# Optimization experiments

Hardware: AMD Instinct MI355X
Metric: run time of the kernel (lower is better)

## Reference

```python
import jax, jax.numpy as jnp
import numpy as np

# pywt db4 reconstruction low-pass (rec_lo) coefficients.
_H = np.array([
    0.23037781330885523, 0.7148465705525415, 0.6308807679295904,
    -0.02798376941698385, -0.18703481171888114, 0.030841381835986965,
    0.032883011666982945, -0.010597401784997278], dtype=np.float64)
# pywt dec_lo = _H[::-1]; conv (flipped) correlation kernel = dec_lo[::-1] = _H.
_FLO = _H
# dec_hi[k] = (-1)^(7-k) * _H[k]; correlation kernel = dec_hi[::-1] -> (-1)^k * _H[7-k].
_FHI = np.array([(-1.0) ** k * _H[7 - k] for k in range(8)])
_FILT = jnp.asarray(np.stack([_FLO, _FHI])[:, None, :], dtype=jnp.float32)  # [2,1,8]
_PAD = 7  # filter_len - 1
_LEVEL = 4


def _dwt_step(sig):
    """One pywt dwt level, mode='symmetric'. sig: [N, L] -> (cA, cD), each [N, (L+7)//2]."""
    # symmetric (half-sample) extension by filter_len-1 each side, drop first sample
    # so that stride-2 VALID correlation reproduces pywt's output phase/length.
    xp = jnp.pad(sig, ((0, 0), (_PAD, _PAD)), mode='symmetric')[:, 1:]
    out = jax.lax.conv_general_dilated(
        xp[:, None, :], _FILT, window_strides=(2,), padding='VALID',
        dimension_numbers=('NCH', 'OIH', 'NCH'))  # [N, 2, (L+7)//2]
    return out[:, 0, :], out[:, 1, :]


def setup_inputs() -> dict:
    key = jax.random.key(0)
    x = jax.random.normal(key, (64, 4096, 32), dtype=jnp.float32)  # [B, L, C]
    return {"x": x}


def reference(x):
    """Faithful batched version of pywt.wavedec(x[i,:,j], 'db4', 'symmetric', level=4).
    Returns tuple (cA4, cD4, cD3, cD2, cD1), each [B, C, scale_len]."""
    B, L, C = x.shape
    sig = jnp.transpose(x, (0, 2, 1)).reshape(B * C, L)
    details = []
    for _ in range(_LEVEL):
        sig, cd = _dwt_step(sig)
        details.append(cd)
    coeffs = [sig] + details[::-1]  # [cA_L, cD_L, ..., cD_1] like pywt.wavedec
    return tuple(c.reshape(B, C, c.shape[-1]) for c in coeffs)
```

## Files before the change

kernel.cpp:

```cpp
#include <hip/hip_runtime.h>


#define NT 256
#define NCHB 4

#define LPX 634
#define LP1 322
#define LP2 166
#define LP3 86
#define CDP1 314
#define CDP2 154
#define CDP3 82
#define CDP4 40
#define CAP4 40

#define L0C 4096
#define L1C 2051
#define L2C 1029
#define L3C 518
#define L4C 262
#define SC 2048

#define OFF_CD4 (SC * L4C)
#define OFF_CD3 (2 * SC * L4C)
#define OFF_CD2 (OFF_CD3 + SC * L3C)
#define OFF_CD1 (OFF_CD2 + SC * L2C)

__device__ __forceinline__ void filt8(
    const float w0, const float w1, const float w2, const float w3,
    const float w4, const float w5, const float w6, const float w7,
    float& a, float& d) {
    constexpr float FLO[8] = {
        0.23037781330885523f,  0.7148465705525415f,  0.6308807679295904f,
        -0.02798376941698385f, -0.18703481171888114f, 0.030841381835986965f,
        0.032883011666982945f, -0.010597401784997278f};
    constexpr float FHI[8] = {
        -0.010597401784997278f, -0.032883011666982945f, 0.030841381835986965f,
        0.18703481171888114f,  -0.02798376941698385f,  -0.6308807679295904f,
        0.7148465705525415f,   -0.23037781330885523f};
    float a0 = FLO[0] * w0;
    a0 = fmaf(FLO[1], w1, a0); a0 = fmaf(FLO[2], w2, a0); a0 = fmaf(FLO[3], w3, a0);
    float a1 = FLO[4] * w4;
    a1 = fmaf(FLO[5], w5, a1); a1 = fmaf(FLO[6], w6, a1); a1 = fmaf(FLO[7], w7, a1);
    a = a0 + a1;
    float d0 = FHI[0] * w0;
    d0 = fmaf(FHI[1], w1, d0); d0 = fmaf(FHI[2], w2, d0); d0 = fmaf(FHI[3], w3, d0);
    float d1 = FHI[4] * w4;
    d1 = fmaf(FHI[5], w5, d1); d1 = fmaf(FHI[6], w6, d1); d1 = fmaf(FHI[7], w7, d1);
    d = d0 + d1;
}

template <int R, bool MG, bool LAST>
__device__ __forceinline__ void level_run(
    const float* __restrict__ src, int PS, int srclo,
    float* __restrict__ dst, int PD, int DL,
    int lo, int hi,
    float* __restrict__ cdbuf, int CDP,
    float* __restrict__ cabuf,
    int c, int slot) {
    static_assert((R & 1) == 0, "R must be even");
    const int span = hi - lo;
    const int nrun = span / R;
    bool tail = false;
    int i0;
    if (slot < nrun) {
        i0 = lo + slot * R;
    } else if (slot == nrun && nrun * R < span) {
        i0 = lo + ((span - R) & ~1);
        tail = (span & 1) != 0;
    } else {
        return;
    }

    const float* rowb = src + c * PS;
    const float2* row2 = reinterpret_cast<const float2*>(rowb);
    const int p = i0 - (srclo >> 1);
    float2 f0 = row2[p], f1 = row2[p + 1], f2 = row2[p + 2];

    float* dbase = LAST ? nullptr : dst + c * PD;
    float* cdbase = cdbuf + c * CDP;
    float* cabase = LAST ? cabuf + c * CAP4 : nullptr;

    float ap = 0.f, dp = 0.f;
#pragma unroll
    for (int r = 0; r < R; ++r) {
        const float2 f3 = row2[p + 3 + r];
        const int i = i0 + r;
        float a, d;
        filt8(f0.x, f0.y, f1.x, f1.y, f2.x, f2.y, f3.x, f3.y, a, d);
        if (r & 1) {
            const int w = i - 1 - lo;
            if constexpr (!LAST)
                *reinterpret_cast<float2*>(dbase + w + 6) = make_float2(ap, a);
            else
                *reinterpret_cast<float2*>(cabase + w) = make_float2(ap, a);
            *reinterpret_cast<float2*>(cdbase + w) = make_float2(dp, d);
        } else {
            ap = a; dp = d;
        }
        if constexpr (MG && !LAST) {
            if (lo == 0 && i < 6) dbase[5 - i] = a;
            if (hi == DL && i >= DL - 7) dbase[(2 * DL - 1 - i) - lo + 6] = a;
        }
        f0 = f1; f1 = f2; f2 = f3;
    }
    if (tail) {
        const int i = hi - 1;
        const float* s = rowb + 6 - srclo;
        float a, d;
        filt8(s[2*i-6], s[2*i-5], s[2*i-4], s[2*i-3],
              s[2*i-2], s[2*i-1], s[2*i],   s[2*i+1], a, d);
        if constexpr (!LAST) {
            dbase[i - lo + 6] = a;
            if constexpr (MG) {
                if (hi == DL && i >= DL - 7) dbase[(2 * DL - 1 - i) - lo + 6] = a;
            }
        } else {
            cabase[i - lo] = a;
        }
        cdbase[i - lo] = d;
    }
}

__device__ __forceinline__ void dump_rows(
    const float* __restrict__ buf, int pitch, int bufLo,
    float* __restrict__ gbase, int rowLen, int ownLo, int ownHi, int tid) {
    const int span = ownHi - ownLo;
    const int n2 = span >> 1;
    const int off = ownLo - bufLo;
#pragma unroll
    for (int c2 = 0; c2 < NCHB; ++c2) {
        const float2* s2 = reinterpret_cast<const float2*>(buf + c2 * pitch + off);
        float* g = gbase + c2 * rowLen + ownLo;
        for (int k = tid; k < n2; k += NT) {
            const float2 v = s2[k];
            g[2 * k] = v.x;
            g[2 * k + 1] = v.y;
        }
        if ((span & 1) && tid == 0) g[span - 1] = buf[c2 * pitch + off + span - 1];
    }
}

template <bool MG>
__device__ __forceinline__ void cascade(
    const float* bx, float* b1, float* b2, float* b3,
    float* cd1, float* cd2, float* cd3, float* cd4, float* ca4,
    float* __restrict__ out, int sigB, int tile, int c, int slot, int tid,
    int lox, int lo1, int hi1, int lo2, int hi2, int lo3, int hi3,
    int lo4, int hi4) {
    const int o1lo = tile ? 264 * tile - 34 : 0;
    const int o1hi = (tile == 7) ? L1C : 264 * tile + 230;
    const int o2lo = tile ? 132 * tile - 10 : 0;
    const int o2hi = (tile == 7) ? L2C : 132 * tile + 122;
    const int o3lo = tile ? 66 * tile - 2 : 0;
    const int o3hi = (tile == 7) ? L3C : 66 * tile + 64;

    level_run<6, MG, false>(bx, LPX, lox, b1, LP1, L1C, lo1, hi1, cd1, CDP1,
                            nullptr, c, slot);
    __syncthreads();

    dump_rows(cd1, CDP1, lo1, out + OFF_CD1 + sigB * L1C, L1C, o1lo, o1hi, tid);
    level_run<4, MG, false>(b1, LP1, lo1, b2, LP2, L2C, lo2, hi2, cd2, CDP2,
                            nullptr, c, slot);
    __syncthreads();

    dump_rows(cd2, CDP2, lo2, out + OFF_CD2 + sigB * L2C, L2C, o2lo, o2hi, tid);
    level_run<2, MG, false>(b2, LP2, lo2, b3, LP3, L3C, lo3, hi3, cd3, CDP3,
                            nullptr, c, slot);
    __syncthreads();

    dump_rows(cd3, CDP3, lo3, out + OFF_CD3 + sigB * L3C, L3C, o3lo, o3hi, tid);
    level_run<2, MG, true>(b3, LP3, lo3, nullptr, 0, L4C, lo4, hi4, cd4, CDP4,
                           ca4, c, slot);
    __syncthreads();

    dump_rows(cd4, CDP4, lo4, out + OFF_CD4 + sigB * L4C, L4C, lo4, hi4, tid);
    dump_rows(ca4, CAP4, lo4, out + sigB * L4C, L4C, lo4, hi4, tid);
}

__global__ __launch_bounds__(NT, 5) void fused_dwt_kernel(
    const float* __restrict__ x, float* __restrict__ out) {
    __shared__ __align__(16) float bx[NCHB * LPX];
    __shared__ __align__(16) float b1[NCHB * LP1];
    __shared__ __align__(16) float b2[NCHB * LP2];
    __shared__ __align__(16) float b3[NCHB * LP3];
    __shared__ __align__(16) float cd1[NCHB * CDP1];
    __shared__ __align__(16) float cd2[NCHB * CDP2];
    __shared__ __align__(16) float cd3[NCHB * CDP3];
    __shared__ __align__(16) float cd4[NCHB * CDP4];
    __shared__ __align__(16) float ca4[NCHB * CAP4];

    const int bid = blockIdx.x;
    const int work = (bid & 7) * 512 + (bid >> 3);
    const int cg = work & 7;
    const int tile = (work >> 3) & 7;
    const int b = work >> 6;

    const int tid = threadIdx.x;
    const int c = tid & 3;
    const int slot = tid >> 2;
    const int c0 = cg * 4;
    const int sigB = b * 32 + c0;

    const int lo4 = 33 * tile, hi4 = min(L4C, lo4 + 33);
    const int lo3 = max(0, 2 * lo4 - 6), hi3 = min(L3C, 2 * hi4);
    const int lo2 = max(0, 2 * lo3 - 6), hi2 = min(L2C, 2 * hi3);
    const int lo1 = max(0, 2 * lo2 - 6), hi1 = min(L1C, 2 * hi2);
    const int lox = max(0, 2 * lo1 - 6), hix = min(L0C, 2 * hi1);

    const float* xb = x + b * (L0C * 32) + c0;
    const int npair = (hix - lox) >> 1;
    for (int q = tid; q < npair; q += NT) {
        const int j = q << 1;
        const int t = lox + j;
        const float4 va = *reinterpret_cast<const float4*>(xb + t * 32);
        const float4 vb = *reinterpret_cast<const float4*>(xb + t * 32 + 32);
        const float av[4] = {va.x, va.y, va.z, va.w};
        const float bv[4] = {vb.x, vb.y, vb.z, vb.w};
#pragma unroll
        for (int hh = 0; hh < NCHB; ++hh)
            *reinterpret_cast<float2*>(bx + hh * LPX + 6 + j) =
                make_float2(av[hh], bv[hh]);
        if (lox == 0 && t < 6) {
#pragma unroll
            for (int hh = 0; hh < NCHB; ++hh) {
                bx[hh * LPX + 5 - t] = av[hh];
                if (t + 1 < 6) bx[hh * LPX + 4 - t] = bv[hh];
            }
        }
        if (hix == L0C && t + 1 >= L0C - 7) {
#pragma unroll
            for (int hh = 0; hh < NCHB; ++hh) {
                if (t >= L0C - 7) bx[hh * LPX + (2 * L0C - 1 - t) - lox + 6] = av[hh];
                bx[hh * LPX + (2 * L0C - 2 - t) - lox + 6] = bv[hh];
            }
        }
    }
    __syncthreads();

    if (tile == 0 || tile == 7)
        cascade<true>(bx, b1, b2, b3, cd1, cd2, cd3, cd4, ca4, out, sigB, tile,
                      c, slot, tid, lox, lo1, hi1, lo2, hi2, lo3, hi3, lo4, hi4);
    else
        cascade<false>(bx, b1, b2, b3, cd1, cd2, cd3, cd4, ca4, out, sigB, tile,
                       c, slot, tid, lox, lo1, hi1, lo2, hi2, lo3, hi3, lo4, hi4);
}

extern "C" void kernel_launch(void* const* d_in, const int* in_sizes, int n_in,
                              void* d_out, int out_size, void* d_ws, size_t ws_size,
                              hipStream_t stream) {
    (void)in_sizes; (void)n_in; (void)d_ws; (void)ws_size; (void)out_size;
    const float* x = (const float*)d_in[0];
    float* out = (float*)d_out;
    fused_dwt_kernel<<<dim3(4096), dim3(NT), 0, stream>>>(x, out);
}
```

Before: 30.11 us.

## Write detail coefficients straight to global memory, dropping LDS staging buffers

Each thread now stores its detail (and final approximation) coefficients directly to global output, guarded by the tile's ownership range. This removes the shared-memory cd/ca staging buffers and the cooperative dump passes, along with the final barrier. Shared memory use per block shrinks, so launch bounds are raised to allow more resident blocks. The trade-off is that global stores become scattered, strided per-thread scalar writes (consecutive threads hit different channel rows) instead of coalesced row copies.

```diff
diff --git a/kernel.cpp b/kernel.cpp
--- a/kernel.cpp
+++ b/kernel.cpp
@@ -8,11 +8,6 @@
 #define LP1 322
 #define LP2 166
 #define LP3 86
-#define CDP1 314
-#define CDP2 154
-#define CDP3 82
-#define CDP4 40
-#define CAP4 40
 
 #define L0C 4096
 #define L1C 2051
@@ -55,8 +50,8 @@
     const float* __restrict__ src, int PS, int srclo,
     float* __restrict__ dst, int PD, int DL,
     int lo, int hi,
-    float* __restrict__ cdbuf, int CDP,
-    float* __restrict__ cabuf,
+    float* __restrict__ gcd, int ownLo, int ownHi,
+    float* __restrict__ gca,
     int c, int slot) {
     static_assert((R & 1) == 0, "R must be even");
     const int span = hi - lo;
@@ -78,29 +73,27 @@
     float2 f0 = row2[p], f1 = row2[p + 1], f2 = row2[p + 2];
 
     float* dbase = LAST ? nullptr : dst + c * PD;
-    float* cdbase = cdbuf + c * CDP;
-    float* cabase = LAST ? cabuf + c * CAP4 : nullptr;
-
-    float ap = 0.f, dp = 0.f;
+
+    float ap = 0.f;
 #pragma unroll
     for (int r = 0; r < R; ++r) {
         const float2 f3 = row2[p + 3 + r];
         const int i = i0 + r;
         float a, d;
         filt8(f0.x, f0.y, f1.x, f1.y, f2.x, f2.y, f3.x, f3.y, a, d);
-        if (r & 1) {
-            const int w = i - 1 - lo;
-            if constexpr (!LAST)
-                *reinterpret_cast<float2*>(dbase + w + 6) = make_float2(ap, a);
+        if (i >= ownLo && i < ownHi) gcd[i] = d;
+        if constexpr (!LAST) {
+            if (r & 1)
+                *reinterpret_cast<float2*>(dbase + (i - 1 - lo) + 6) =
+                    make_float2(ap, a);
             else
-                *reinterpret_cast<float2*>(cabase + w) = make_float2(ap, a);
-            *reinterpret_cast<float2*>(cdbase + w) = make_float2(dp, d);
+                ap = a;
+            if constexpr (MG) {
+                if (lo == 0 && i < 6) dbase[5 - i] = a;
+                if (hi == DL && i >= DL - 7) dbase[(2 * DL - 1 - i) - lo + 6] = a;
+            }
         } else {
-            ap = a; dp = d;
-        }
-        if constexpr (MG && !LAST) {
-            if (lo == 0 && i < 6) dbase[5 - i] = a;
-            if (hi == DL && i >= DL - 7) dbase[(2 * DL - 1 - i) - lo + 6] = a;
+            gca[i] = a;
         }
         f0 = f1; f1 = f2; f2 = f3;
     }
@@ -110,42 +103,22 @@
         float a, d;
         filt8(s[2*i-6], s[2*i-5], s[2*i-4], s[2*i-3],
               s[2*i-2], s[2*i-1], s[2*i],   s[2*i+1], a, d);
+        if (i >= ownLo && i < ownHi) gcd[i] = d;
         if constexpr (!LAST) {
             dbase[i - lo + 6] = a;
             if constexpr (MG) {
                 if (hi == DL && i >= DL - 7) dbase[(2 * DL - 1 - i) - lo + 6] = a;
             }
         } else {
-            cabase[i - lo] = a;
-        }
-        cdbase[i - lo] = d;
-    }
-}
-
-__device__ __forceinline__ void dump_rows(
-    const float* __restrict__ buf, int pitch, int bufLo,
-    float* __restrict__ gbase, int rowLen, int ownLo, int ownHi, int tid) {
-    const int span = ownHi - ownLo;
-    const int n2 = span >> 1;
-    const int off = ownLo - bufLo;
-#pragma unroll
-    for (int c2 = 0; c2 < NCHB; ++c2) {
-        const float2* s2 = reinterpret_cast<const float2*>(buf + c2 * pitch + off);
-        float* g = gbase + c2 * rowLen + ownLo;
-        for (int k = tid; k < n2; k += NT) {
-            const float2 v = s2[k];
-            g[2 * k] = v.x;
-            g[2 * k + 1] = v.y;
-        }
-        if ((span & 1) && tid == 0) g[span - 1] = buf[c2 * pitch + off + span - 1];
+            gca[i] = a;
+        }
     }
 }
 
 template <bool MG>
 __device__ __forceinline__ void cascade(
     const float* bx, float* b1, float* b2, float* b3,
-    float* cd1, float* cd2, float* cd3, float* cd4, float* ca4,
-    float* __restrict__ out, int sigB, int tile, int c, int slot, int tid,
+    float* __restrict__ out, int sigB, int tile, int c, int slot,
     int lox, int lo1, int hi1, int lo2, int hi2, int lo3, int hi3,
     int lo4, int hi4) {
     const int o1lo = tile ? 264 * tile - 34 : 0;
@@ -155,40 +128,35 @@
     const int o3lo = tile ? 66 * tile - 2 : 0;
     const int o3hi = (tile == 7) ? L3C : 66 * tile + 64;
 
-    level_run<6, MG, false>(bx, LPX, lox, b1, LP1, L1C, lo1, hi1, cd1, CDP1,
-                            nullptr, c, slot);
-    __syncthreads();
-
-    dump_rows(cd1, CDP1, lo1, out + OFF_CD1 + sigB * L1C, L1C, o1lo, o1hi, tid);
-    level_run<4, MG, false>(b1, LP1, lo1, b2, LP2, L2C, lo2, hi2, cd2, CDP2,
-                            nullptr, c, slot);
-    __syncthreads();
-
-    dump_rows(cd2, CDP2, lo2, out + OFF_CD2 + sigB * L2C, L2C, o2lo, o2hi, tid);
-    level_run<2, MG, false>(b2, LP2, lo2, b3, LP3, L3C, lo3, hi3, cd3, CDP3,
-                            nullptr, c, slot);
-    __syncthreads();
-
-    dump_rows(cd3, CDP3, lo3, out + OFF_CD3 + sigB * L3C, L3C, o3lo, o3hi, tid);
-    level_run<2, MG, true>(b3, LP3, lo3, nullptr, 0, L4C, lo4, hi4, cd4, CDP4,
-                           ca4, c, slot);
-    __syncthreads();
-
-    dump_rows(cd4, CDP4, lo4, out + OFF_CD4 + sigB * L4C, L4C, lo4, hi4, tid);
-    dump_rows(ca4, CAP4, lo4, out + sigB * L4C, L4C, lo4, hi4, tid);
-}
-
-__global__ __launch_bounds__(NT, 5) void fused_dwt_kernel(
+    const int sig = sigB + c;
+    float* gcd1 = out + OFF_CD1 + sig * L1C;
+    float* gcd2 = out + OFF_CD2 + sig * L2C;
+    float* gcd3 = out + OFF_CD3 + sig * L3C;
+    float* gcd4 = out + OFF_CD4 + sig * L4C;
+    float* gca4 = out + sig * L4C;
+
+    level_run<6, MG, false>(bx, LPX, lox, b1, LP1, L1C, lo1, hi1,
+                            gcd1, o1lo, o1hi, nullptr, c, slot);
+    __syncthreads();
+
+    level_run<4, MG, false>(b1, LP1, lo1, b2, LP2, L2C, lo2, hi2,
+                            gcd2, o2lo, o2hi, nullptr, c, slot);
+    __syncthreads();
+
+    level_run<2, MG, false>(b2, LP2, lo2, b3, LP3, L3C, lo3, hi3,
+                            gcd3, o3lo, o3hi, nullptr, c, slot);
+    __syncthreads();
+
+    level_run<2, false, true>(b3, LP3, lo3, nullptr, 0, L4C, lo4, hi4,
+                              gcd4, lo4, hi4, gca4, c, slot);
+}
+
+__global__ __launch_bounds__(NT, 8) void fused_dwt_kernel(
     const float* __restrict__ x, float* __restrict__ out) {
     __shared__ __align__(16) float bx[NCHB * LPX];
     __shared__ __align__(16) float b1[NCHB * LP1];
     __shared__ __align__(16) float b2[NCHB * LP2];
     __shared__ __align__(16) float b3[NCHB * LP3];
-    __shared__ __align__(16) float cd1[NCHB * CDP1];
-    __shared__ __align__(16) float cd2[NCHB * CDP2];
-    __shared__ __align__(16) float cd3[NCHB * CDP3];
-    __shared__ __align__(16) float cd4[NCHB * CDP4];
-    __shared__ __align__(16) float ca4[NCHB * CAP4];
 
     const int bid = blockIdx.x;
     const int work = (bid & 7) * 512 + (bid >> 3);
@@ -239,11 +207,11 @@
     __syncthreads();
 
     if (tile == 0 || tile == 7)
-        cascade<true>(bx, b1, b2, b3, cd1, cd2, cd3, cd4, ca4, out, sigB, tile,
-                      c, slot, tid, lox, lo1, hi1, lo2, hi2, lo3, hi3, lo4, hi4);
+        cascade<true>(bx, b1, b2, b3, out, sigB, tile, c, slot,
+                      lox, lo1, hi1, lo2, hi2, lo3, hi3, lo4, hi4);
     else
-        cascade<false>(bx, b1, b2, b3, cd1, cd2, cd3, cd4, ca4, out, sigB, tile,
-                       c, slot, tid, lox, lo1, hi1, lo2, hi2, lo3, hi3, lo4, hi4);
+        cascade<false>(bx, b1, b2, b3, out, sigB, tile, c, slot,
+                       lox, lo1, hi1, lo2, hi2, lo3, hi3, lo4, hi4);
 }
 
 extern "C" void kernel_launch(void* const* d_in, const int* in_sizes, int n_in,
```

Result: no change. 30.50 us (+1.3%).
